# Kernel optimization log

Hardware: AMD Instinct MI355X
Metric: run time of the kernel (lower is better)

The kernel has to match this reference:

```python
import jax, jax.numpy as jnp
import numpy as np

N_NODES = 100000
N_EDGES = 3200000
K_HOPS = 10
ALPHA = 0.1


def setup_inputs() -> dict:
    key = jax.random.key(0)
    ks = jax.random.split(key, 7)
    x = jax.random.normal(ks[0], (N_NODES, 500), dtype=jnp.float32)
    edge_index = jax.random.randint(ks[1], (2, N_EDGES), 0, N_NODES, dtype=jnp.int32)
    W1 = jax.random.normal(ks[2], (500, 64), dtype=jnp.float32) * 0.05
    b1 = jax.random.normal(ks[3], (64,), dtype=jnp.float32) * 0.05
    W2 = jax.random.normal(ks[4], (64, 64), dtype=jnp.float32) * 0.1
    b2 = jax.random.normal(ks[5], (64,), dtype=jnp.float32) * 0.05
    # PPR init: temp[k] = alpha*(1-alpha)^k, temp[K] = (1-alpha)^K
    temp = ALPHA * (1.0 - ALPHA) ** np.arange(K_HOPS + 1)
    temp[-1] = (1.0 - ALPHA) ** K_HOPS
    temp = jnp.asarray(temp, dtype=jnp.float32)
    return {"x": x, "edge_index": edge_index, "W1": W1, "b1": b1,
            "W2": W2, "b2": b2, "temp": temp}


def reference(x, edge_index, W1, b1, W2, b2, temp):
    n = x.shape[0]
    # MLP (dropout is identity in eval mode)
    h = jax.nn.relu(x @ W1 + b1)
    h = h @ W2 + b2  # [N, C]

    # gcn_norm with self-loops (edge_weight=None -> all ones)
    loops = jnp.arange(n, dtype=edge_index.dtype)
    row = jnp.concatenate([edge_index[0], loops])  # source (x_j)
    col = jnp.concatenate([edge_index[1], loops])  # target (aggregate)
    w = jnp.ones(row.shape[0], dtype=h.dtype)
    deg = jax.ops.segment_sum(w, col, num_segments=n)
    dinv = jnp.where(deg > 0, jax.lax.rsqrt(deg), 0.0)
    norm = dinv[row] * w * dinv[col]  # [E+N]

    # GPR propagation: hidden = sum_k temp[k] * A_hat^k h
    hidden = h * temp[0]
    cur = h
    for k in range(K_HOPS):
        cur = jax.ops.segment_sum(norm[:, None] * cur[row], col, num_segments=n)
        hidden = hidden + temp[k + 1] * cur

    return jax.nn.log_softmax(hidden, axis=1)
```

## Files before the change

kernel.cpp:

```cpp
#include <hip/hip_runtime.h>
#include <hip/hip_bf16.h>
#include <math.h>

#define FEAT_IN 500
#define HID 64
#define MT_PER_WAVE 2
#define NPB 128
#define MAXB 1024

typedef unsigned int uint;
typedef unsigned short ushort;
typedef __attribute__((ext_vector_type(8))) short bf16x8;
typedef __attribute__((ext_vector_type(4))) float f32x4;

__device__ inline ushort f2bf(float f) {
    uint u = __float_as_uint(f);
    uint r = (u + 0x7fff + ((u >> 16) & 1)) >> 16;
    return (ushort)r;
}

__device__ inline uint pk2(float a, float b) {
    uint ua = __float_as_uint(a), ub = __float_as_uint(b);
    ua = ua + 0x7fff + ((ua >> 16) & 1);
    ub = ub + 0x7fff + ((ub >> 16) & 1);
    return (ua >> 16) | (ub & 0xffff0000u);
}

__device__ inline void bf8_unpack(const uint4 v, float f[8]) {
    f[0] = __uint_as_float(v.x << 16);
    f[1] = __uint_as_float(v.x & 0xffff0000u);
    f[2] = __uint_as_float(v.y << 16);
    f[3] = __uint_as_float(v.y & 0xffff0000u);
    f[4] = __uint_as_float(v.z << 16);
    f[5] = __uint_as_float(v.z & 0xffff0000u);
    f[6] = __uint_as_float(v.w << 16);
    f[7] = __uint_as_float(v.w & 0xffff0000u);
}

__global__ __launch_bounds__(256) void bcnt_kernel(const int* __restrict__ col,
                                                   int* __restrict__ bcnt, int E, int nbkt) {
    __shared__ int cnt[MAXB];
    int tid = threadIdx.x;
    for (int j = tid; j < nbkt; j += 256) cnt[j] = 0;
    __syncthreads();
    int stride = gridDim.x * 256;
    for (int e = blockIdx.x * 256 + tid; e < E; e += stride) {
        atomicAdd(&cnt[col[e] >> 7], 1);
    }
    __syncthreads();
    for (int j = tid; j < nbkt; j += 256) {
        int v = cnt[j];
        if (v) atomicAdd(&bcnt[j], v);
    }
}

__global__ void bscan_kernel(const int* __restrict__ bcnt, int* __restrict__ boff,
                             int* __restrict__ bcur, int* __restrict__ ptr,
                             int nbkt, int n, int E) {
    int lane = threadIdx.x;
    int run = 0;
    for (int base = 0; base < nbkt; base += 64) {
        int i = base + lane;
        int v = (i < nbkt) ? bcnt[i] : 0;
        int sc = v;
#pragma unroll
        for (int d = 1; d < 64; d <<= 1) {
            int t = __shfl_up(sc, d);
            if (lane >= d) sc += t;
        }
        if (i < nbkt) {
            int ex = run + sc - v;
            boff[i] = ex;
            bcur[i] = ex;
        }
        run += __shfl(sc, 63);
    }
    if (lane == 0) {
        boff[nbkt] = E;
        ptr[n] = E;
    }
}

__global__ __launch_bounds__(1024) void bscat_kernel(const int* __restrict__ row,
                                                     const int* __restrict__ col,
                                                     int* __restrict__ bcur,
                                                     uint* __restrict__ csr_tmp,
                                                     int E, int nbkt) {
    __shared__ int cnt[MAXB];
    __shared__ int pos[MAXB];
    int tid = threadIdx.x;
    int chunk = (E + gridDim.x - 1) / gridDim.x;
    int c0 = blockIdx.x * chunk;
    int c1 = min(E, c0 + chunk);
    for (int j = tid; j < nbkt; j += 1024) cnt[j] = 0;
    __syncthreads();
    for (int e = c0 + tid; e < c1; e += 1024) atomicAdd(&cnt[col[e] >> 7], 1);
    __syncthreads();
    for (int j = tid; j < nbkt; j += 1024) {
        int v = cnt[j];
        pos[j] = v ? atomicAdd(&bcur[j], v) : 0;
    }
    __syncthreads();
    for (int e = c0 + tid; e < c1; e += 1024) {
        int c = col[e];
        int j = c >> 7;
        int r = atomicAdd(&pos[j], 1);
        csr_tmp[r] = ((uint)row[e] << 7) | (uint)(c & (NPB - 1));
    }
}

__global__ __launch_bounds__(256) void bsort_kernel(const uint* __restrict__ csr_tmp,
                                                    const int* __restrict__ boff,
                                                    int* __restrict__ ptr,
                                                    float* __restrict__ dinv,
                                                    int* __restrict__ csr_src,
                                                    int n) {
    __shared__ int degl[NPB];
    __shared__ int offl[NPB];
    int b = blockIdx.x;
    int tid = threadIdx.x;
    int t0 = boff[b], t1 = boff[b + 1];
    if (tid < NPB) degl[tid] = 0;
    __syncthreads();
    for (int p = t0 + tid; p < t1; p += 256) {
        uint pk = csr_tmp[p];
        atomicAdd(&degl[pk & (NPB - 1)], 1);
    }
    __syncthreads();
    if (tid < 64) {
        int v0 = degl[tid];
        int s0 = v0;
#pragma unroll
        for (int d = 1; d < 64; d <<= 1) {
            int t = __shfl_up(s0, d);
            if (tid >= d) s0 += t;
        }
        int tot0 = __shfl(s0, 63);
        int v1 = degl[64 + tid];
        int s1 = v1;
#pragma unroll
        for (int d = 1; d < 64; d <<= 1) {
            int t = __shfl_up(s1, d);
            if (tid >= d) s1 += t;
        }
        offl[tid] = s0 - v0;
        offl[64 + tid] = tot0 + s1 - v1;
    }
    __syncthreads();
    if (tid < NPB) {
        int node = b * NPB + tid;
        if (node < n) {
            ptr[node] = t0 + offl[tid];
            dinv[node] = rsqrtf((float)(degl[tid] + 1));
        }
    }
    __syncthreads();
    for (int p = t0 + tid; p < t1; p += 256) {
        uint pk = csr_tmp[p];
        int l = pk & (NPB - 1);
        int r = t0 + atomicAdd(&offl[l], 1);
        csr_src[r] = (int)(pk >> 7);
    }
}

__global__ void swz_kernel(const float* __restrict__ W1, const float* __restrict__ W2,
                           ushort* __restrict__ w1s, ushort* __restrict__ w2s) {
    int idx = blockIdx.x * blockDim.x + threadIdx.x;
    if (idx < 32768) {
        int j = idx & 7;
        int l = (idx >> 3) & 63;
        int t = (idx >> 9) & 3;
        int c = idx >> 11;
        int k = c * 32 + (l >> 4) * 8 + j;
        int nn = t * 16 + (l & 15);
        float v = (k < FEAT_IN) ? W1[(size_t)k * HID + nn] : 0.0f;
        w1s[idx] = f2bf(v);
    } else if (idx < 32768 + 4096) {
        int r = idx - 32768;
        int j = r & 7;
        int l = (r >> 3) & 63;
        int t = (r >> 9) & 3;
        int c = r >> 11;
        int k = c * 32 + (l >> 4) * 8 + j;
        int nn = t * 16 + (l & 15);
        w2s[r] = f2bf(W2[(size_t)k * HID + nn]);
    }
}

__global__ __launch_bounds__(256) void mlp_kernel(const float* __restrict__ x,
                                                  const ushort* __restrict__ w1s,
                                                  const float* __restrict__ b1,
                                                  const ushort* __restrict__ w2s,
                                                  const float* __restrict__ b2,
                                                  const float* __restrict__ temp,
                                                  const float* __restrict__ dinv,
                                                  ushort* __restrict__ A,
                                                  float* __restrict__ out, int n) {
    __shared__ ushort hls[4][16 * 72];
    const int lane = threadIdx.x & 63;
    const int wv = threadIdx.x >> 6;
    const int g = lane >> 4;
    const int c15 = lane & 15;
    const int nmt = (n + 15) / 16;
    int mt0 = (blockIdx.x * 4 + wv) * MT_PER_WAVE;
    if (mt0 >= nmt) return;

    float b1v[4], b2v[4];
#pragma unroll
    for (int t = 0; t < 4; t++) {
        b1v[t] = b1[t * 16 + c15];
        b2v[t] = b2[t * 16 + c15];
    }
    float t0 = temp[0];
    ushort* hl = hls[wv];

    for (int m = 0; m < MT_PER_WAVE; m++) {
        int mt = mt0 + m;
        if (mt >= nmt) break;
        int row = mt * 16 + c15;
        const float* xr = x + (size_t)row * FEAT_IN;
        bool rok = (row < n);

        f32x4 acc[4] = {{0.f, 0.f, 0.f, 0.f}, {0.f, 0.f, 0.f, 0.f},
                        {0.f, 0.f, 0.f, 0.f}, {0.f, 0.f, 0.f, 0.f}};

        for (int c = 0; c < 15; c++) {
            int k = c * 32 + g * 8;
            float4 lo = {0.f, 0.f, 0.f, 0.f}, hi = {0.f, 0.f, 0.f, 0.f};
            if (rok) {
                lo = *(const float4*)(xr + k);
                hi = *(const float4*)(xr + k + 4);
            }
            uint4 au;
            au.x = pk2(lo.x, lo.y);
            au.y = pk2(lo.z, lo.w);
            au.z = pk2(hi.x, hi.y);
            au.w = pk2(hi.z, hi.w);
            bf16x8 a = *(bf16x8*)&au;
            const ushort* wp = w1s + ((size_t)c * 4) * 512 + lane * 8;
#pragma unroll
            for (int t = 0; t < 4; t++) {
                bf16x8 b = *(const bf16x8*)(wp + t * 512);
                acc[t] = __builtin_amdgcn_mfma_f32_16x16x32_bf16(a, b, acc[t], 0, 0, 0);
            }
        }
        {
            float v[8];
#pragma unroll
            for (int j = 0; j < 8; j++) {
                int k = 480 + g * 8 + j;
                v[j] = (rok && k < FEAT_IN) ? xr[k] : 0.0f;
            }
            uint4 au;
            au.x = pk2(v[0], v[1]);
            au.y = pk2(v[2], v[3]);
            au.z = pk2(v[4], v[5]);
            au.w = pk2(v[6], v[7]);
            bf16x8 a = *(bf16x8*)&au;
            const ushort* wp = w1s + (size_t)15 * 4 * 512 + lane * 8;
#pragma unroll
            for (int t = 0; t < 4; t++) {
                bf16x8 b = *(const bf16x8*)(wp + t * 512);
                acc[t] = __builtin_amdgcn_mfma_f32_16x16x32_bf16(a, b, acc[t], 0, 0, 0);
            }
        }

#pragma unroll
        for (int t = 0; t < 4; t++) {
#pragma unroll
            for (int r = 0; r < 4; r++) {
                float h = fmaxf(acc[t][r] + b1v[t], 0.0f);
                hl[(g * 4 + r) * 72 + t * 16 + c15] = f2bf(h);
            }
        }

        f32x4 acc2[4] = {{0.f, 0.f, 0.f, 0.f}, {0.f, 0.f, 0.f, 0.f},
                         {0.f, 0.f, 0.f, 0.f}, {0.f, 0.f, 0.f, 0.f}};
#pragma unroll
        for (int c2 = 0; c2 < 2; c2++) {
            bf16x8 a2 = *(const bf16x8*)(hl + c15 * 72 + c2 * 32 + g * 8);
            const ushort* wp2 = w2s + ((size_t)c2 * 4) * 512 + lane * 8;
#pragma unroll
            for (int t = 0; t < 4; t++) {
                bf16x8 b = *(const bf16x8*)(wp2 + t * 512);
                acc2[t] = __builtin_amdgcn_mfma_f32_16x16x32_bf16(a2, b, acc2[t], 0, 0, 0);
            }
        }

        float dvr[4];
#pragma unroll
        for (int r = 0; r < 4; r++) {
            int orow = mt * 16 + g * 4 + r;
            dvr[r] = (orow < n) ? dinv[orow] : 0.0f;
        }
#pragma unroll
        for (int t = 0; t < 4; t++) {
#pragma unroll
            for (int r = 0; r < 4; r++) {
                int orow = mt * 16 + g * 4 + r;
                if (orow < n) {
                    float d = acc2[t][r] + b2v[t];
                    size_t o = (size_t)orow * HID + t * 16 + c15;
                    A[o] = f2bf(dvr[r] * d);
                    out[o] = t0 * d;
                }
            }
        }
    }
}

__global__ __launch_bounds__(256) void hop_kernel(const int* __restrict__ ptr,
                                                  const int* __restrict__ csr_src,
                                                  const float* __restrict__ dinv,
                                                  const ushort* __restrict__ cur,
                                                  ushort* __restrict__ nxt,
                                                  float* __restrict__ out,
                                                  const float* __restrict__ temp,
                                                  int tidx, int n) {
    int i = (blockIdx.x * blockDim.x + threadIdx.x) >> 6;
    int lane = threadIdx.x & 63;
    if (i >= n) return;
    const int g = lane >> 3;
    const int q = lane & 7;

    int s = ptr[i];
    int e = ptr[i + 1];
    const uint* curu = (const uint*)cur;

    float acc[8] = {0.f, 0.f, 0.f, 0.f, 0.f, 0.f, 0.f, 0.f};
    float accB[8] = {0.f, 0.f, 0.f, 0.f, 0.f, 0.f, 0.f, 0.f};

    int p = s;
    for (; p + 16 <= e; p += 16) {
        int j0 = csr_src[p + g];
        int j1 = csr_src[p + 8 + g];
        uint4 v0 = *(const uint4*)(curu + (size_t)j0 * 32 + q * 4);
        uint4 v1 = *(const uint4*)(curu + (size_t)j1 * 32 + q * 4);
        float f0[8], f1[8];
        bf8_unpack(v0, f0);
        bf8_unpack(v1, f1);
#pragma unroll
        for (int t = 0; t < 8; t++) acc[t] += f0[t];
#pragma unroll
        for (int t = 0; t < 8; t++) accB[t] += f1[t];
    }
    for (; p < e; p += 8) {
        int pe = p + g;
        bool ok = pe < e;
        int pc = ok ? pe : (e - 1);
        int j = csr_src[pc];
        float w = ok ? 1.0f : 0.0f;
        uint4 v = *(const uint4*)(curu + (size_t)j * 32 + q * 4);
        float f[8];
        bf8_unpack(v, f);
#pragma unroll
        for (int t = 0; t < 8; t++) acc[t] += w * f[t];
    }
#pragma unroll
    for (int t = 0; t < 8; t++) acc[t] += accB[t];

#pragma unroll
    for (int m = 8; m <= 32; m <<= 1) {
#pragma unroll
        for (int t = 0; t < 8; t++) acc[t] += __shfl_xor(acc[t], m);
    }

    uint4 sv = *(const uint4*)(curu + (size_t)i * 32 + q * 4);
    float sf[8];
    bf8_unpack(sv, sf);
#pragma unroll
    for (int t = 0; t < 8; t++) acc[t] += sf[t];

    if (lane < 8) {
        float d = dinv[i];
        float dd = d * d;
        float tk = temp[tidx] * d;
        uint4 pk;
        pk.x = (uint)f2bf(dd * acc[0]) | ((uint)f2bf(dd * acc[1]) << 16);
        pk.y = (uint)f2bf(dd * acc[2]) | ((uint)f2bf(dd * acc[3]) << 16);
        pk.z = (uint)f2bf(dd * acc[4]) | ((uint)f2bf(dd * acc[5]) << 16);
        pk.w = (uint)f2bf(dd * acc[6]) | ((uint)f2bf(dd * acc[7]) << 16);
        *(uint4*)((uint*)nxt + (size_t)i * 32 + q * 4) = pk;

        float* op = out + (size_t)i * HID + q * 8;
        float4 o0 = *(const float4*)(op);
        float4 o1 = *(const float4*)(op + 4);
        o0.x += tk * acc[0]; o0.y += tk * acc[1]; o0.z += tk * acc[2]; o0.w += tk * acc[3];
        o1.x += tk * acc[4]; o1.y += tk * acc[5]; o1.z += tk * acc[6]; o1.w += tk * acc[7];
        *(float4*)(op) = o0;
        *(float4*)(op + 4) = o1;
    }
}

__global__ __launch_bounds__(256) void lsm_kernel(float* __restrict__ out, int n) {
    int i = (blockIdx.x * blockDim.x + threadIdx.x) >> 6;
    int lane = threadIdx.x & 63;
    if (i >= n) return;
    size_t o = (size_t)i * HID + lane;
    float v = out[o];
    float m = v;
#pragma unroll
    for (int d = 32; d >= 1; d >>= 1) m = fmaxf(m, __shfl_xor(m, d));
    float ex = expf(v - m);
#pragma unroll
    for (int d = 32; d >= 1; d >>= 1) ex += __shfl_xor(ex, d);
    out[o] = v - m - logf(ex);
}

extern "C" void kernel_launch(void* const* d_in, const int* in_sizes, int n_in,
                              void* d_out, int out_size, void* d_ws, size_t ws_size,
                              hipStream_t stream) {
    const float* x    = (const float*)d_in[0];
    const int*   ei   = (const int*)d_in[1];
    const float* W1   = (const float*)d_in[2];
    const float* b1   = (const float*)d_in[3];
    const float* W2   = (const float*)d_in[4];
    const float* b2   = (const float*)d_in[5];
    const float* temp = (const float*)d_in[6];

    int n = in_sizes[0] / FEAT_IN;
    int E = in_sizes[1] / 2;
    int K = in_sizes[6] - 1;
    const int* row = ei;
    const int* col = ei + E;
    int nbkt = (n + NPB - 1) >> 7;

    char* ws = (char*)d_ws;
    size_t off = 0;
    auto alloc = [&](size_t bytes) -> void* {
        void* p = (void*)(ws + off);
        off += (bytes + 255) & ~(size_t)255;
        return p;
    };
    size_t nf = (size_t)n * HID;
    ushort* A      = (ushort*)alloc(nf * sizeof(ushort));
    ushort* B      = (ushort*)alloc(nf * sizeof(ushort));
    float* dinv    = (float*)alloc((size_t)n * sizeof(float));
    int*   ptr     = (int*)alloc((size_t)(n + 1) * sizeof(int));
    int*   bcnt    = (int*)alloc((size_t)MAXB * sizeof(int));
    int*   boff    = (int*)alloc((size_t)(MAXB + 1) * sizeof(int));
    int*   bcur    = (int*)alloc((size_t)MAXB * sizeof(int));
    uint*  csr_tmp = (uint*)alloc((size_t)E * sizeof(uint));
    int*   csr_src = (int*)alloc((size_t)E * sizeof(int));
    ushort* w1s    = (ushort*)alloc(32768 * sizeof(ushort));
    ushort* w2s    = (ushort*)alloc(4096 * sizeof(ushort));
    (void)ws_size;

    float* out = (float*)d_out;

    hipMemsetAsync(bcnt, 0, (size_t)nbkt * sizeof(int), stream);

    bcnt_kernel<<<256, 256, 0, stream>>>(col, bcnt, E, nbkt);
    bscan_kernel<<<1, 64, 0, stream>>>(bcnt, boff, bcur, ptr, nbkt, n, E);
    bscat_kernel<<<256, 1024, 0, stream>>>(row, col, bcur, csr_tmp, E, nbkt);
    bsort_kernel<<<nbkt, 256, 0, stream>>>(csr_tmp, boff, ptr, dinv, csr_src, n);
    swz_kernel<<<(32768 + 4096 + 255) / 256, 256, 0, stream>>>(W1, W2, w1s, w2s);

    int nmt = (n + 15) / 16;
    int mlp_blocks = (nmt + 4 * MT_PER_WAVE - 1) / (4 * MT_PER_WAVE);
    mlp_kernel<<<mlp_blocks, 256, 0, stream>>>(x, w1s, b1, w2s, b2, temp, dinv, A, out, n);

    int hop_blocks = (n + 3) / 4;
    ushort* cur = A;
    ushort* nxt = B;
    for (int k = 0; k < K; k++) {
        hop_kernel<<<hop_blocks, 256, 0, stream>>>(ptr, csr_src, dinv, cur, nxt, out,
                                                   temp, k + 1, n);
        ushort* t = cur; cur = nxt; nxt = t;
    }

    lsm_kernel<<<hop_blocks, 256, 0, stream>>>(out, n);
}
```

Before: 1.086 ms.

## Split propagation features into four 16-column tiles for cache-local gathers

The bf16 feature matrices move from a row-major [N,64] layout to four column tiles of [N,16]. Each hop block now handles one tile, and block indices are interleaved so that neighbouring blocks cover the same node group across tiles. A wave now gathers 32 neighbours per step with 32-byte reads, so each tile's working set (about 3.2 MB) fits in cache, in exchange for more blocks and repeated CSR index reads. MT_PER_WAVE in the MLP kernel also drops from 2 to 1.

```diff
diff --git a/kernel.cpp b/kernel.cpp
--- a/kernel.cpp
+++ b/kernel.cpp
@@ -4,9 +4,10 @@
 
 #define FEAT_IN 500
 #define HID 64
-#define MT_PER_WAVE 2
+#define MT_PER_WAVE 1
 #define NPB 128
 #define MAXB 1024
+#define NTILE 4
 
 typedef unsigned int uint;
 typedef unsigned short ushort;
@@ -300,78 +301,75 @@
                 int orow = mt * 16 + g * 4 + r;
                 if (orow < n) {
                     float d = acc2[t][r] + b2v[t];
-                    size_t o = (size_t)orow * HID + t * 16 + c15;
-                    A[o] = f2bf(dvr[r] * d);
-                    out[o] = t0 * d;
+                    A[(size_t)t * n * 16 + (size_t)orow * 16 + c15] = f2bf(dvr[r] * d);
+                    out[(size_t)orow * HID + t * 16 + c15] = t0 * d;
                 }
             }
         }
     }
 }
 
-__global__ __launch_bounds__(256) void hop_kernel(const int* __restrict__ ptr,
-                                                  const int* __restrict__ csr_src,
-                                                  const float* __restrict__ dinv,
-                                                  const ushort* __restrict__ cur,
-                                                  ushort* __restrict__ nxt,
-                                                  float* __restrict__ out,
-                                                  const float* __restrict__ temp,
-                                                  int tidx, int n) {
-    int i = (blockIdx.x * blockDim.x + threadIdx.x) >> 6;
+__global__ __launch_bounds__(256) void hopt_kernel(const int* __restrict__ ptr,
+                                                   const int* __restrict__ csr_src,
+                                                   const float* __restrict__ dinv,
+                                                   const ushort* __restrict__ cur,
+                                                   ushort* __restrict__ nxt,
+                                                   float* __restrict__ out,
+                                                   const float* __restrict__ temp,
+                                                   int tidx, int n) {
+    int b = blockIdx.x;
+    int tile = (b & 7) >> 1;
+    int ngrp = (b >> 3) * 2 + (b & 1);
+    int wv = threadIdx.x >> 6;
     int lane = threadIdx.x & 63;
+    int i = ngrp * 4 + wv;
     if (i >= n) return;
-    const int g = lane >> 3;
-    const int q = lane & 7;
+    const int g = lane >> 1;
+    const int q = lane & 1;
+
+    size_t tbase = (size_t)tile * n * 16;
+    const uint* curu = (const uint*)(cur + tbase);
 
     int s = ptr[i];
     int e = ptr[i + 1];
-    const uint* curu = (const uint*)cur;
 
     float acc[8] = {0.f, 0.f, 0.f, 0.f, 0.f, 0.f, 0.f, 0.f};
-    float accB[8] = {0.f, 0.f, 0.f, 0.f, 0.f, 0.f, 0.f, 0.f};
 
     int p = s;
-    for (; p + 16 <= e; p += 16) {
-        int j0 = csr_src[p + g];
-        int j1 = csr_src[p + 8 + g];
-        uint4 v0 = *(const uint4*)(curu + (size_t)j0 * 32 + q * 4);
-        uint4 v1 = *(const uint4*)(curu + (size_t)j1 * 32 + q * 4);
-        float f0[8], f1[8];
-        bf8_unpack(v0, f0);
-        bf8_unpack(v1, f1);
-#pragma unroll
-        for (int t = 0; t < 8; t++) acc[t] += f0[t];
-#pragma unroll
-        for (int t = 0; t < 8; t++) accB[t] += f1[t];
-    }
-    for (; p < e; p += 8) {
+    for (; p + 32 <= e; p += 32) {
+        int j = csr_src[p + g];
+        uint4 v = *(const uint4*)(curu + (size_t)j * 8 + q * 4);
+        float f[8];
+        bf8_unpack(v, f);
+#pragma unroll
+        for (int t = 0; t < 8; t++) acc[t] += f[t];
+    }
+    if (p < e) {
         int pe = p + g;
         bool ok = pe < e;
         int pc = ok ? pe : (e - 1);
         int j = csr_src[pc];
         float w = ok ? 1.0f : 0.0f;
-        uint4 v = *(const uint4*)(curu + (size_t)j * 32 + q * 4);
+        uint4 v = *(const uint4*)(curu + (size_t)j * 8 + q * 4);
         float f[8];
         bf8_unpack(v, f);
 #pragma unroll
         for (int t = 0; t < 8; t++) acc[t] += w * f[t];
     }
-#pragma unroll
-    for (int t = 0; t < 8; t++) acc[t] += accB[t];
-
-#pragma unroll
-    for (int m = 8; m <= 32; m <<= 1) {
+
+#pragma unroll
+    for (int m = 2; m <= 32; m <<= 1) {
 #pragma unroll
         for (int t = 0; t < 8; t++) acc[t] += __shfl_xor(acc[t], m);
     }
 
-    uint4 sv = *(const uint4*)(curu + (size_t)i * 32 + q * 4);
+    uint4 sv = *(const uint4*)(curu + (size_t)i * 8 + q * 4);
     float sf[8];
     bf8_unpack(sv, sf);
 #pragma unroll
     for (int t = 0; t < 8; t++) acc[t] += sf[t];
 
-    if (lane < 8) {
+    if (lane < 2) {
         float d = dinv[i];
         float dd = d * d;
         float tk = temp[tidx] * d;
@@ -380,9 +378,9 @@
         pk.y = (uint)f2bf(dd * acc[2]) | ((uint)f2bf(dd * acc[3]) << 16);
         pk.z = (uint)f2bf(dd * acc[4]) | ((uint)f2bf(dd * acc[5]) << 16);
         pk.w = (uint)f2bf(dd * acc[6]) | ((uint)f2bf(dd * acc[7]) << 16);
-        *(uint4*)((uint*)nxt + (size_t)i * 32 + q * 4) = pk;
-
-        float* op = out + (size_t)i * HID + q * 8;
+        *(uint4*)((uint*)(nxt + tbase) + (size_t)i * 8 + q * 4) = pk;
+
+        float* op = out + (size_t)i * HID + tile * 16 + q * 8;
         float4 o0 = *(const float4*)(op);
         float4 o1 = *(const float4*)(op + 4);
         o0.x += tk * acc[0]; o0.y += tk * acc[1]; o0.z += tk * acc[2]; o0.w += tk * acc[3];
@@ -460,14 +458,17 @@
     int mlp_blocks = (nmt + 4 * MT_PER_WAVE - 1) / (4 * MT_PER_WAVE);
     mlp_kernel<<<mlp_blocks, 256, 0, stream>>>(x, w1s, b1, w2s, b2, temp, dinv, A, out, n);
 
-    int hop_blocks = (n + 3) / 4;
+    int ngroups = (n + 3) / 4;
+    int gh = (ngroups + 1) / 2;
+    int hop_blocks = 8 * gh;
     ushort* cur = A;
     ushort* nxt = B;
     for (int k = 0; k < K; k++) {
-        hop_kernel<<<hop_blocks, 256, 0, stream>>>(ptr, csr_src, dinv, cur, nxt, out,
-                                                   temp, k + 1, n);
+        hopt_kernel<<<hop_blocks, 256, 0, stream>>>(ptr, csr_src, dinv, cur, nxt, out,
+                                                    temp, k + 1, n);
         ushort* t = cur; cur = nxt; nxt = t;
     }
 
-    lsm_kernel<<<hop_blocks, 256, 0, stream>>>(out, n);
-}
+    int lsm_blocks = (n + 3) / 4;
+    lsm_kernel<<<lsm_blocks, 256, 0, stream>>>(out, n);
+}
```

Result: slower. 2.123 ms (+95.5%).
